# Kernel tuning notes

Hardware: AMD Instinct MI355X
Metric: run time of the kernel (lower is better)

The kernel has to match this reference:

```python
import jax, jax.numpy as jnp
import numpy as np

BIG_NUMBER = 1000000.0


def setup_inputs() -> dict:
    key = jax.random.key(0)
    ks = jax.random.split(key, 20)
    B, N, F, MID, OUT = 2, 512, 128, 128, 128
    node_fts = jax.random.normal(ks[0], (B, N, F), jnp.float32)
    edge_fts = jax.random.normal(ks[1], (B, N, N, F), jnp.float32)
    graph_fts = jax.random.normal(ks[2], (B, F), jnp.float32)
    hidden = jax.random.normal(ks[3], (B, N, F), jnp.float32)
    # Bernoulli(0.5) adjacency + self-loops so masked max is always valid
    adj = (jax.random.uniform(ks[4], (B, N, N)) < 0.5).astype(jnp.float32)
    adj = jnp.maximum(adj, jnp.eye(N, dtype=jnp.float32)[None])
    Z = 2 * F  # z = cat(node_fts, hidden)

    def lin(k, fan_in, fan_out):
        kw, kb = jax.random.split(k)
        lim = 1.0 / np.sqrt(fan_in)
        W = jax.random.uniform(kw, (fan_in, fan_out), jnp.float32, -lim, lim)
        b = jax.random.uniform(kb, (fan_out,), jnp.float32, -lim, lim)
        return W, b

    W1, b1 = lin(ks[5], Z, MID)
    W2, b2 = lin(ks[6], Z, MID)
    We, be = lin(ks[7], F, MID)
    Wg, bg = lin(ks[8], F, MID)
    Wo1, bo1 = lin(ks[9], Z, OUT)
    Wo2, bo2 = lin(ks[10], MID, OUT)
    return dict(node_fts=node_fts, edge_fts=edge_fts, graph_fts=graph_fts,
                adj_mat=adj, hidden=hidden,
                W1=W1, b1=b1, W2=W2, b2=b2, We=We, be=be, Wg=Wg, bg=bg,
                Wo1=Wo1, bo1=bo1, Wo2=Wo2, bo2=bo2)


def reference(node_fts, edge_fts, graph_fts, adj_mat, hidden,
              W1, b1, W2, b2, We, be, Wg, bg, Wo1, bo1, Wo2, bo2):
    # z: (B, N, 2F)
    z = jnp.concatenate([node_fts, hidden], axis=-1)
    msg_1 = z @ W1 + b1                      # (B, N, mid) - sender
    msg_2 = z @ W2 + b2                      # (B, N, mid) - receiver
    msg_e = edge_fts @ We + be               # (B, N, N, mid)
    msg_g = graph_fts @ Wg + bg              # (B, mid)
    # msgs[b, i, j] = msg_1[b, j] + msg_2[b, i] + msg_e[b, i, j] + msg_g[b]
    msgs = (msg_1[:, None, :, :] + msg_2[:, :, None, :]
            + msg_e + msg_g[:, None, None, :])  # (B, N, N, mid)
    # masked max over axis 1 (senders in the torch reduction dim=1)
    maxarg = jnp.where(adj_mat[..., None] > 0, msgs, -BIG_NUMBER)
    msgs_red = jnp.max(maxarg, axis=1)       # (B, N, mid)
    h_1 = z @ Wo1 + bo1
    h_2 = msgs_red @ Wo2 + bo2
    ret = jax.nn.relu(h_1 + h_2)             # (B, N, out)
    return ret
```

## Files before the change

kernel.cpp:

```cpp
#include <hip/hip_runtime.h>


typedef __bf16 bf16x8 __attribute__((ext_vector_type(8)));
typedef float  f32x4  __attribute__((ext_vector_type(4)));

#define MFMA16(a,b,c) __builtin_amdgcn_mfma_f32_16x16x32_bf16(a,b,c,0,0,0)

union BFrag { bf16x8 v; unsigned short s[8]; unsigned u[4]; };

__device__ __forceinline__ unsigned packbf(float lo, float hi){
  return __builtin_amdgcn_perm(__builtin_bit_cast(unsigned, hi),
                               __builtin_bit_cast(unsigned, lo), 0x07060302u);
}
__device__ __forceinline__ unsigned short f2bt(float f){
  return (unsigned short)(__builtin_bit_cast(unsigned, f) >> 16);
}
__device__ __forceinline__ unsigned short f2b(float f){
  unsigned u = __builtin_bit_cast(unsigned, f);
  u = u + 0x7FFFu + ((u >> 16) & 1u);
  return (unsigned short)(u >> 16);
}

#define WS_MS2  0
#define WS_MS1  131072
#define WS_H1   262144
#define WS_MSGG 393216
#define WS_PART 393472

__global__ __launch_bounds__(64) void k1_small(
    const float* __restrict__ node,
    const float* __restrict__ hidden,
    const float* __restrict__ graph,
    const float* __restrict__ W1, const float* __restrict__ b1,
    const float* __restrict__ W2, const float* __restrict__ b2,
    const float* __restrict__ Wo1,const float* __restrict__ bo1,
    const float* __restrict__ Wg, const float* __restrict__ bg,
    float* __restrict__ ws)
{
  int bid  = blockIdx.x;
  int lane = threadIdx.x;
  int col = lane & 15, quad = lane >> 4;

  if (bid < 192) {
    int mat = bid >> 6;
    int rt  = bid & 63;
    int r0  = rt * 16;
    const float* W  = (mat==0) ? W1 : (mat==1) ? W2 : Wo1;
    const float* bb = (mat==0) ? b1 : (mat==1) ? b2 : bo1;
    float* dst = ws + ((mat==0) ? WS_MS1 : (mat==1) ? WS_MS2 : WS_H1);

    bf16x8 a[8];
    long rowb = (long)(r0 + col) * 128;
#pragma unroll
    for (int kk = 0; kk < 8; ++kk) {
      const float* src = (kk < 4) ? node : hidden;
      int f = (kk & 3) * 32 + quad * 8;
      f32x4 v0 = *(const f32x4*)(src + rowb + f);
      f32x4 v1 = *(const f32x4*)(src + rowb + f + 4);
      BFrag t;
      t.u[0] = packbf(v0[0], v0[1]); t.u[1] = packbf(v0[2], v0[3]);
      t.u[2] = packbf(v1[0], v1[1]); t.u[3] = packbf(v1[2], v1[3]);
      a[kk] = t.v;
    }
    f32x4 acc[8];
#pragma unroll
    for (int nt = 0; nt < 8; ++nt) acc[nt] = (f32x4)0.f;
#pragma unroll
    for (int kk = 0; kk < 8; ++kk) {
      BFrag bf[8];
#pragma unroll
      for (int nt = 0; nt < 8; ++nt)
#pragma unroll
        for (int j = 0; j < 8; ++j)
          bf[nt].s[j] = f2bt(W[(kk*32 + quad*8 + j)*128 + nt*16 + col]);
#pragma unroll
      for (int nt = 0; nt < 8; ++nt) acc[nt] = MFMA16(a[kk], bf[nt].v, acc[nt]);
    }
#pragma unroll
    for (int nt = 0; nt < 8; ++nt) {
      float bv = bb[nt*16 + col];
#pragma unroll
      for (int r = 0; r < 4; ++r) {
        int row = r0 + quad*4 + r;
        dst[(long)row*128 + nt*16 + col] = acc[nt][r] + bv;
      }
    }
  } else {
    int b = bid - 192;
    float a0 = 0.f, a1 = 0.f;
    for (int k = 0; k < 128; ++k) {
      float g = graph[b*128 + k];
      a0 += g * Wg[k*128 + lane];
      a1 += g * Wg[k*128 + 64 + lane];
    }
    ws[WS_MSGG + b*128 + lane]      = a0 + bg[lane];
    ws[WS_MSGG + b*128 + 64 + lane] = a1 + bg[64 + lane];
  }
}

#define LDS_PITCH 136

__global__ __launch_bounds__(256, 2) void k2_main(
    const float* __restrict__ E,
    const float* __restrict__ We,
    const float* __restrict__ adj,
    const float* __restrict__ msg2,
    float* __restrict__ part)
{
  __shared__ alignas(16) unsigned short smem[LDS_PITCH * 128];

  int bid = blockIdx.x;
  int jt = bid & 31, s = (bid >> 5) & 7, b = bid >> 8;
  int tid = threadIdx.x;
  int w = tid >> 6, lane = tid & 63;
  int col = lane & 15, quad = lane >> 4;
  int j0 = jt * 16;

#pragma unroll
  for (int p = 0; p < 8; ++p) {
    int g = p*2048 + tid*8;
    int k = g >> 7, m = g & 127;
    f32x4 v0 = *(const f32x4*)(We + k*128 + m);
    f32x4 v1 = *(const f32x4*)(We + k*128 + m + 4);
    unsigned short sv[8] = { f2b(v0[0]), f2b(v0[1]), f2b(v0[2]), f2b(v0[3]),
                             f2b(v1[0]), f2b(v1[1]), f2b(v1[2]), f2b(v1[3]) };
#pragma unroll
    for (int e = 0; e < 8; ++e) smem[(m+e)*LDS_PITCH + k] = sv[e];
  }
  __syncthreads();

  f32x4 mx[8];
#pragma unroll
  for (int nt = 0; nt < 8; ++nt) mx[nt] = (f32x4)(-1.0e6f);

  int i0 = s*64 + w*16;

  f32x4 rv[8]; float4 av; float m2[8];
  {
    const float* ep = E + ((long)(b*512 + i0)*512 + j0 + col)*128;
#pragma unroll
    for (int kk = 0; kk < 4; ++kk) {
      rv[2*kk]   = *(const f32x4*)(ep + kk*32 + quad*8);
      rv[2*kk+1] = *(const f32x4*)(ep + kk*32 + quad*8 + 4);
    }
    av = *(const float4*)(adj + (long)(b*512 + i0)*512 + j0 + quad*4);
    const float* mp = msg2 + (long)(b*512 + i0)*128 + col;
#pragma unroll
    for (int nt = 0; nt < 8; ++nt) m2[nt] = mp[nt*16];
  }

#pragma unroll 1
  for (int ii = 0; ii < 16; ++ii) {
    int inx = i0 + ((ii < 15) ? ii + 1 : ii);

    f32x4 nrv[8]; float4 nav; float nm2[8];
    {
      const float* ep = E + ((long)(b*512 + inx)*512 + j0 + col)*128;
#pragma unroll
      for (int kk = 0; kk < 4; ++kk) {
        nrv[2*kk]   = *(const f32x4*)(ep + kk*32 + quad*8);
        nrv[2*kk+1] = *(const f32x4*)(ep + kk*32 + quad*8 + 4);
      }
      nav = *(const float4*)(adj + (long)(b*512 + inx)*512 + j0 + quad*4);
      const float* mp = msg2 + (long)(b*512 + inx)*128 + col;
#pragma unroll
      for (int nt = 0; nt < 8; ++nt) nm2[nt] = mp[nt*16];
    }

    BFrag a[4];
#pragma unroll
    for (int kk = 0; kk < 4; ++kk) {
      a[kk].u[0] = packbf(rv[2*kk][0],   rv[2*kk][1]);
      a[kk].u[1] = packbf(rv[2*kk][2],   rv[2*kk][3]);
      a[kk].u[2] = packbf(rv[2*kk+1][0], rv[2*kk+1][1]);
      a[kk].u[3] = packbf(rv[2*kk+1][2], rv[2*kk+1][3]);
    }

    f32x4 biasv;
    biasv[0] = av.x*1.0e6f - 1.0e6f;
    biasv[1] = av.y*1.0e6f - 1.0e6f;
    biasv[2] = av.z*1.0e6f - 1.0e6f;
    biasv[3] = av.w*1.0e6f - 1.0e6f;

    f32x4 T[8];
#pragma unroll
    for (int nt = 0; nt < 8; ++nt) T[nt] = biasv + m2[nt];
#pragma unroll
    for (int kk = 0; kk < 4; ++kk)
#pragma unroll
      for (int nt = 0; nt < 8; ++nt) {
        bf16x8 bb = *(const bf16x8*)(&smem[(nt*16 + col)*LDS_PITCH + kk*32 + quad*8]);
        T[nt] = MFMA16(a[kk].v, bb, T[nt]);
      }
#pragma unroll
    for (int nt = 0; nt < 8; ++nt)
#pragma unroll
      for (int r = 0; r < 4; ++r)
        mx[nt][r] = fmaxf(mx[nt][r], T[nt][r]);

#pragma unroll
    for (int q = 0; q < 8; ++q) rv[q] = nrv[q];
    av = nav;
#pragma unroll
    for (int nt = 0; nt < 8; ++nt) m2[nt] = nm2[nt];
  }

  __syncthreads();
  float* red = (float*)smem;
#pragma unroll
  for (int nt = 0; nt < 8; ++nt)
#pragma unroll
    for (int r = 0; r < 4; ++r)
      red[(w*16 + quad*4 + r)*128 + nt*16 + col] = mx[nt][r];
  __syncthreads();
  {
    int e0 = tid * 8;
    const f32x4* r4 = (const f32x4*)red;
    f32x4 v0 = r4[e0 >> 2], v1 = r4[(e0 >> 2) + 1];
#pragma unroll
    for (int ww = 1; ww < 4; ++ww) {
      f32x4 u0 = r4[(ww*2048 + e0) >> 2];
      f32x4 u1 = r4[((ww*2048 + e0) >> 2) + 1];
#pragma unroll
      for (int r = 0; r < 4; ++r) { v0[r] = fmaxf(v0[r], u0[r]); v1[r] = fmaxf(v1[r], u1[r]); }
    }
    f32x4* pp = (f32x4*)(part + ((long)((b*32 + jt)*8 + s))*2048 + e0);
    pp[0] = v0; pp[1] = v1;
  }
}

__global__ __launch_bounds__(64) void k3_out(
    const float* __restrict__ ws,
    const float* __restrict__ Wo2,
    const float* __restrict__ be,
    const float* __restrict__ bo2,
    float* __restrict__ out)
{
  int bid = blockIdx.x;
  int b = bid >> 5, jt = bid & 31, j0 = jt * 16;
  int lane = threadIdx.x, col = lane & 15, quad = lane >> 4;

  const float* part = ws + WS_PART + ((long)((b*32 + jt)*8))*2048;
  const float* msg1 = ws + WS_MS1;
  const float* msgg = ws + WS_MSGG + b*128;
  const float* h1   = ws + WS_H1;

  BFrag af[4];
#pragma unroll
  for (int kk = 0; kk < 4; ++kk) {
    int off = kk*32 + quad*8;
    const float* p0 = part + col*128 + off;
    f32x4 v0 = *(const f32x4*)(p0);
    f32x4 v1 = *(const f32x4*)(p0 + 4);
#pragma unroll
    for (int s = 1; s < 8; ++s) {
      f32x4 u0 = *(const f32x4*)(p0 + s*2048);
      f32x4 u1 = *(const f32x4*)(p0 + s*2048 + 4);
#pragma unroll
      for (int r = 0; r < 4; ++r) { v0[r] = fmaxf(v0[r], u0[r]); v1[r] = fmaxf(v1[r], u1[r]); }
    }
    const float* m1 = msg1 + (long)(b*512 + j0 + col)*128 + off;
    f32x4 w0 = *(const f32x4*)m1, w1 = *(const f32x4*)(m1 + 4);
#pragma unroll
    for (int r = 0; r < 4; ++r) {
      float g0 = msgg[off + r]     + be[off + r];
      float g1 = msgg[off + 4 + r] + be[off + 4 + r];
      af[kk].s[r]     = f2b(v0[r] + w0[r] + g0);
      af[kk].s[4 + r] = f2b(v1[r] + w1[r] + g1);
    }
  }

  f32x4 acc[8];
#pragma unroll
  for (int nt = 0; nt < 8; ++nt) acc[nt] = (f32x4)0.f;
#pragma unroll
  for (int kk = 0; kk < 4; ++kk) {
    BFrag bf[8];
#pragma unroll
    for (int nt = 0; nt < 8; ++nt)
#pragma unroll
      for (int j = 0; j < 8; ++j)
        bf[nt].s[j] = f2bt(Wo2[(kk*32 + quad*8 + j)*128 + nt*16 + col]);
#pragma unroll
    for (int nt = 0; nt < 8; ++nt) acc[nt] = MFMA16(af[kk].v, bf[nt].v, acc[nt]);
  }

#pragma unroll
  for (int nt = 0; nt < 8; ++nt) {
    float bv = bo2[nt*16 + col];
#pragma unroll
    for (int r = 0; r < 4; ++r) {
      int row = j0 + quad*4 + r;
      long idx = (long)(b*512 + row)*128 + nt*16 + col;
      float v = h1[idx] + acc[nt][r] + bv;
      out[idx] = v < 0.f ? 0.f : v;
    }
  }
}

extern "C" void kernel_launch(void* const* d_in, const int* in_sizes, int n_in,
                              void* d_out, int out_size, void* d_ws, size_t ws_size,
                              hipStream_t stream)
{
  const float* node   = (const float*)d_in[0];
  const float* E      = (const float*)d_in[1];
  const float* graph  = (const float*)d_in[2];
  const float* adj    = (const float*)d_in[3];
  const float* hidden = (const float*)d_in[4];
  const float* W1  = (const float*)d_in[5];
  const float* b1  = (const float*)d_in[6];
  const float* W2  = (const float*)d_in[7];
  const float* b2  = (const float*)d_in[8];
  const float* We  = (const float*)d_in[9];
  const float* be  = (const float*)d_in[10];
  const float* Wg  = (const float*)d_in[11];
  const float* bg  = (const float*)d_in[12];
  const float* Wo1 = (const float*)d_in[13];
  const float* bo1 = (const float*)d_in[14];
  const float* Wo2 = (const float*)d_in[15];
  const float* bo2 = (const float*)d_in[16];
  float* ws  = (float*)d_ws;
  float* out = (float*)d_out;

  hipLaunchKernelGGL(k1_small, dim3(194), dim3(64), 0, stream,
                     node, hidden, graph, W1, b1, W2, b2, Wo1, bo1, Wg, bg, ws);
  hipLaunchKernelGGL(k2_main, dim3(512), dim3(256), 0, stream,
                     E, We, adj, ws + WS_MS2, ws + WS_PART);
  hipLaunchKernelGGL(k3_out, dim3(64), dim3(64), 0, stream,
                     ws, Wo2, be, bo2, out);
}
```

Before: 422.3 us.

## Stream edge features via async global-to-LDS loads with register-resident We fragments

Result: no change. 430.7 us (+2.0%).

```diff
diff --git a/kernel.cpp b/kernel.cpp
--- a/kernel.cpp
+++ b/kernel.cpp
@@ -20,12 +20,19 @@
   u = u + 0x7FFFu + ((u >> 16) & 1u);
   return (unsigned short)(u >> 16);
 }
+__device__ __forceinline__ float b2f(unsigned short u){
+  unsigned v = ((unsigned)u) << 16;
+  return __builtin_bit_cast(float, v);
+}
+
+#define WAITVM(N) asm volatile("s_waitcnt vmcnt(" #N ")" ::: "memory")
 
 #define WS_MS2  0
 #define WS_MS1  131072
 #define WS_H1   262144
 #define WS_MSGG 393216
 #define WS_PART 393472
+#define WS_WEFR 4587776
 
 __global__ __launch_bounds__(64) void k1_small(
     const float* __restrict__ node,
@@ -35,6 +42,7 @@
     const float* __restrict__ W2, const float* __restrict__ b2,
     const float* __restrict__ Wo1,const float* __restrict__ bo1,
     const float* __restrict__ Wg, const float* __restrict__ bg,
+    const float* __restrict__ We,
     float* __restrict__ ws)
 {
   int bid  = blockIdx.x;
@@ -85,7 +93,7 @@
         dst[(long)row*128 + nt*16 + col] = acc[nt][r] + bv;
       }
     }
-  } else {
+  } else if (bid < 194) {
     int b = bid - 192;
     float a0 = 0.f, a1 = 0.f;
     for (int k = 0; k < 128; ++k) {
@@ -95,138 +103,141 @@
     }
     ws[WS_MSGG + b*128 + lane]      = a0 + bg[lane];
     ws[WS_MSGG + b*128 + 64 + lane] = a1 + bg[64 + lane];
-  }
-}
-
-#define LDS_PITCH 136
-
-__global__ __launch_bounds__(256, 2) void k2_main(
+  } else {
+    unsigned short* wf = (unsigned short*)(ws + WS_WEFR);
+#pragma unroll
+    for (int kk = 0; kk < 4; ++kk)
+#pragma unroll
+      for (int nt = 0; nt < 8; ++nt) {
+        BFrag t;
+#pragma unroll
+        for (int e = 0; e < 8; ++e)
+          t.s[e] = f2b(We[(kk*32 + quad*8 + e)*128 + nt*16 + col]);
+        *(bf16x8*)(wf + ((kk*8 + nt)*64 + lane)*8) = t.v;
+      }
+  }
+}
+
+__device__ __forceinline__ void issue_slice(const float* ei, void* lbase, int lane){
+  int l5 = lane >> 5, s5 = lane & 31;
+#pragma unroll
+  for (int inst = 0; inst < 8; ++inst) {
+    int j = inst*2 + l5;
+    const float* gp = ei + j*128 + ((s5 ^ j) << 2);
+    __builtin_amdgcn_global_load_lds(
+        (const __attribute__((address_space(1))) void*)gp,
+        (__attribute__((address_space(3))) void*)((char*)lbase + inst*1024),
+        16, 0, 0);
+  }
+}
+
+__global__ __launch_bounds__(64, 1) void k2_main(
     const float* __restrict__ E,
-    const float* __restrict__ We,
     const float* __restrict__ adj,
     const float* __restrict__ msg2,
+    const unsigned short* __restrict__ wefrag,
     float* __restrict__ part)
 {
-  __shared__ alignas(16) unsigned short smem[LDS_PITCH * 128];
-
-  int bid = blockIdx.x;
-  int jt = bid & 31, s = (bid >> 5) & 7, b = bid >> 8;
-  int tid = threadIdx.x;
-  int w = tid >> 6, lane = tid & 63;
-  int col = lane & 15, quad = lane >> 4;
-  int j0 = jt * 16;
+  __shared__ alignas(16) unsigned char lds_raw[4*8192 + 4096 + 512];
+  unsigned short* const m2l  = (unsigned short*)(lds_raw + 32768);
+  unsigned short* const adjl = (unsigned short*)(lds_raw + 32768 + 4096);
+
+  const int bid = blockIdx.x;
+  const int jt = bid & 31, s = (bid >> 5) & 31, b = bid >> 10;
+  const int lane = threadIdx.x;
+  const int col = lane & 15, quad = lane >> 4;
+  const int i0 = s * 16, j0 = jt * 16;
+
+  const float* Eb = E + ((long)(b*512 + i0)*512 + j0) * 128;
+
+  bf16x8 bfr[4][8];
+#pragma unroll
+  for (int kk = 0; kk < 4; ++kk)
+#pragma unroll
+    for (int nt = 0; nt < 8; ++nt)
+      bfr[kk][nt] = *(const bf16x8*)(wefrag + ((kk*8 + nt)*64 + lane)*8);
 
 #pragma unroll
   for (int p = 0; p < 8; ++p) {
-    int g = p*2048 + tid*8;
-    int k = g >> 7, m = g & 127;
-    f32x4 v0 = *(const f32x4*)(We + k*128 + m);
-    f32x4 v1 = *(const f32x4*)(We + k*128 + m + 4);
-    unsigned short sv[8] = { f2b(v0[0]), f2b(v0[1]), f2b(v0[2]), f2b(v0[3]),
-                             f2b(v1[0]), f2b(v1[1]), f2b(v1[2]), f2b(v1[3]) };
-#pragma unroll
-    for (int e = 0; e < 8; ++e) smem[(m+e)*LDS_PITCH + k] = sv[e];
+    int f = p*256 + lane*4;
+    const float* mp = msg2 + (long)(b*512 + i0 + (f >> 7))*128 + (f & 127);
+    f32x4 v = *(const f32x4*)mp;
+    uint2 uu;
+    uu.x = (unsigned)f2b(v[0]) | ((unsigned)f2b(v[1]) << 16);
+    uu.y = (unsigned)f2b(v[2]) | ((unsigned)f2b(v[3]) << 16);
+    *(uint2*)(m2l + f) = uu;
+  }
+  {
+    int row = lane >> 2, c4 = (lane & 3) * 4;
+    f32x4 v = *(const f32x4*)(adj + (long)(b*512 + i0 + row)*512 + j0 + c4);
+    uint2 uu;
+    uu.x = (unsigned)f2bt(v[0]) | ((unsigned)f2bt(v[1]) << 16);
+    uu.y = (unsigned)f2bt(v[2]) | ((unsigned)f2bt(v[3]) << 16);
+    *(uint2*)(adjl + row*16 + c4) = uu;
   }
   __syncthreads();
 
+#pragma unroll
+  for (int d = 0; d < 4; ++d)
+    issue_slice(Eb + (long)d*65536, lds_raw + d*8192, lane);
+
   f32x4 mx[8];
 #pragma unroll
   for (int nt = 0; nt < 8; ++nt) mx[nt] = (f32x4)(-1.0e6f);
 
-  int i0 = s*64 + w*16;
-
-  f32x4 rv[8]; float4 av; float m2[8];
-  {
-    const float* ep = E + ((long)(b*512 + i0)*512 + j0 + col)*128;
+  auto body = [&](int ii) {
+    const float* sl = (const float*)(lds_raw + (ii & 3) * 8192);
+    BFrag a[4];
 #pragma unroll
     for (int kk = 0; kk < 4; ++kk) {
-      rv[2*kk]   = *(const f32x4*)(ep + kk*32 + quad*8);
-      rv[2*kk+1] = *(const f32x4*)(ep + kk*32 + quad*8 + 4);
-    }
-    av = *(const float4*)(adj + (long)(b*512 + i0)*512 + j0 + quad*4);
-    const float* mp = msg2 + (long)(b*512 + i0)*128 + col;
-#pragma unroll
-    for (int nt = 0; nt < 8; ++nt) m2[nt] = mp[nt*16];
-  }
-
-#pragma unroll 1
-  for (int ii = 0; ii < 16; ++ii) {
-    int inx = i0 + ((ii < 15) ? ii + 1 : ii);
-
-    f32x4 nrv[8]; float4 nav; float nm2[8];
-    {
-      const float* ep = E + ((long)(b*512 + inx)*512 + j0 + col)*128;
-#pragma unroll
-      for (int kk = 0; kk < 4; ++kk) {
-        nrv[2*kk]   = *(const f32x4*)(ep + kk*32 + quad*8);
-        nrv[2*kk+1] = *(const f32x4*)(ep + kk*32 + quad*8 + 4);
-      }
-      nav = *(const float4*)(adj + (long)(b*512 + inx)*512 + j0 + quad*4);
-      const float* mp = msg2 + (long)(b*512 + inx)*128 + col;
-#pragma unroll
-      for (int nt = 0; nt < 8; ++nt) nm2[nt] = mp[nt*16];
-    }
-
-    BFrag a[4];
-#pragma unroll
-    for (int kk = 0; kk < 4; ++kk) {
-      a[kk].u[0] = packbf(rv[2*kk][0],   rv[2*kk][1]);
-      a[kk].u[1] = packbf(rv[2*kk][2],   rv[2*kk][3]);
-      a[kk].u[2] = packbf(rv[2*kk+1][0], rv[2*kk+1][1]);
-      a[kk].u[3] = packbf(rv[2*kk+1][2], rv[2*kk+1][3]);
-    }
-
+      int cb = kk*8 + quad*2;
+      f32x4 v0 = *(const f32x4*)(sl + col*128 + ((cb    ) ^ col)*4);
+      f32x4 v1 = *(const f32x4*)(sl + col*128 + ((cb + 1) ^ col)*4);
+      a[kk].u[0] = packbf(v0[0], v0[1]); a[kk].u[1] = packbf(v0[2], v0[3]);
+      a[kk].u[2] = packbf(v1[0], v1[1]); a[kk].u[3] = packbf(v1[2], v1[3]);
+    }
+    float m2[8];
+#pragma unroll
+    for (int nt = 0; nt < 8; ++nt) m2[nt] = b2f(m2l[ii*128 + nt*16 + col]);
+    ushort4 av = *(const ushort4*)(adjl + ii*16 + quad*4);
     f32x4 biasv;
-    biasv[0] = av.x*1.0e6f - 1.0e6f;
-    biasv[1] = av.y*1.0e6f - 1.0e6f;
-    biasv[2] = av.z*1.0e6f - 1.0e6f;
-    biasv[3] = av.w*1.0e6f - 1.0e6f;
-
+    biasv[0] = b2f(av.x)*1.0e6f - 1.0e6f;
+    biasv[1] = b2f(av.y)*1.0e6f - 1.0e6f;
+    biasv[2] = b2f(av.z)*1.0e6f - 1.0e6f;
+    biasv[3] = b2f(av.w)*1.0e6f - 1.0e6f;
     f32x4 T[8];
 #pragma unroll
     for (int nt = 0; nt < 8; ++nt) T[nt] = biasv + m2[nt];
 #pragma unroll
     for (int kk = 0; kk < 4; ++kk)
 #pragma unroll
-      for (int nt = 0; nt < 8; ++nt) {
-        bf16x8 bb = *(const bf16x8*)(&smem[(nt*16 + col)*LDS_PITCH + kk*32 + quad*8]);
-        T[nt] = MFMA16(a[kk].v, bb, T[nt]);
-      }
+      for (int nt = 0; nt < 8; ++nt)
+        T[nt] = MFMA16(a[kk].v, bfr[kk][nt], T[nt]);
 #pragma unroll
     for (int nt = 0; nt < 8; ++nt)
 #pragma unroll
       for (int r = 0; r < 4; ++r)
         mx[nt][r] = fmaxf(mx[nt][r], T[nt][r]);
-
-#pragma unroll
-    for (int q = 0; q < 8; ++q) rv[q] = nrv[q];
-    av = nav;
-#pragma unroll
-    for (int nt = 0; nt < 8; ++nt) m2[nt] = nm2[nt];
-  }
-
-  __syncthreads();
-  float* red = (float*)smem;
+  };
+
+#pragma unroll 1
+  for (int ii = 0; ii < 12; ++ii) {
+    WAITVM(24);
+    body(ii);
+    asm volatile("" ::: "memory");
+    issue_slice(Eb + (long)(ii+4)*65536, lds_raw + (ii & 3)*8192, lane);
+  }
+  WAITVM(24); body(12);
+  WAITVM(16); body(13);
+  WAITVM(8);  body(14);
+  WAITVM(0);  body(15);
+
+  float* pp = part + ((long)((b*32 + jt)*32 + s)) * 2048;
 #pragma unroll
   for (int nt = 0; nt < 8; ++nt)
 #pragma unroll
     for (int r = 0; r < 4; ++r)
-      red[(w*16 + quad*4 + r)*128 + nt*16 + col] = mx[nt][r];
-  __syncthreads();
-  {
-    int e0 = tid * 8;
-    const f32x4* r4 = (const f32x4*)red;
-    f32x4 v0 = r4[e0 >> 2], v1 = r4[(e0 >> 2) + 1];
-#pragma unroll
-    for (int ww = 1; ww < 4; ++ww) {
-      f32x4 u0 = r4[(ww*2048 + e0) >> 2];
-      f32x4 u1 = r4[((ww*2048 + e0) >> 2) + 1];
-#pragma unroll
-      for (int r = 0; r < 4; ++r) { v0[r] = fmaxf(v0[r], u0[r]); v1[r] = fmaxf(v1[r], u1[r]); }
-    }
-    f32x4* pp = (f32x4*)(part + ((long)((b*32 + jt)*8 + s))*2048 + e0);
-    pp[0] = v0; pp[1] = v1;
-  }
+      pp[(quad*4 + r)*128 + nt*16 + col] = mx[nt][r];
 }
 
 __global__ __launch_bounds__(64) void k3_out(
@@ -240,7 +251,7 @@
   int b = bid >> 5, jt = bid & 31, j0 = jt * 16;
   int lane = threadIdx.x, col = lane & 15, quad = lane >> 4;
 
-  const float* part = ws + WS_PART + ((long)((b*32 + jt)*8))*2048;
+  const float* part = ws + WS_PART + ((long)((b*32 + jt)*32))*2048;
   const float* msg1 = ws + WS_MS1;
   const float* msgg = ws + WS_MSGG + b*128;
   const float* h1   = ws + WS_H1;
@@ -253,7 +264,7 @@
     f32x4 v0 = *(const f32x4*)(p0);
     f32x4 v1 = *(const f32x4*)(p0 + 4);
 #pragma unroll
-    for (int s = 1; s < 8; ++s) {
+    for (int s = 1; s < 32; ++s) {
       f32x4 u0 = *(const f32x4*)(p0 + s*2048);
       f32x4 u1 = *(const f32x4*)(p0 + s*2048 + 4);
 #pragma unroll
@@ -322,10 +333,11 @@
   float* ws  = (float*)d_ws;
   float* out = (float*)d_out;
 
-  hipLaunchKernelGGL(k1_small, dim3(194), dim3(64), 0, stream,
-                     node, hidden, graph, W1, b1, W2, b2, Wo1, bo1, Wg, bg, ws);
-  hipLaunchKernelGGL(k2_main, dim3(512), dim3(256), 0, stream,
-                     E, We, adj, ws + WS_MS2, ws + WS_PART);
+  hipLaunchKernelGGL(k1_small, dim3(195), dim3(64), 0, stream,
+                     node, hidden, graph, W1, b1, W2, b2, Wo1, bo1, Wg, bg, We, ws);
+  hipLaunchKernelGGL(k2_main, dim3(2048), dim3(64), 0, stream,
+                     E, adj, ws + WS_MS2, (const unsigned short*)(ws + WS_WEFR),
+                     ws + WS_PART);
   hipLaunchKernelGGL(k3_out, dim3(64), dim3(64), 0, stream,
                      ws, Wo2, be, bo2, out);
 }
```
